# Performance work log

Hardware: AMD Instinct MI355X
Metric: run time of the kernel (lower is better)

Reference implementation:

```python
import jax, jax.numpy as jnp
import numpy as np


def setup_inputs() -> dict:
    key = jax.random.key(0)
    kx, kw = jax.random.split(key)
    B, IN, OUT = 8192, 1024, 4096
    x = jax.random.normal(kx, (B, IN), dtype=jnp.float32)
    # torch.rand -> uniform [0,1)
    weight = jax.random.uniform(kw, (IN, OUT), dtype=jnp.float32)
    return {"x": x, "weight": weight}


def reference(x, weight):
    # Faithful to: (x.unsqueeze(-1) - weight).pow(2).sum(-2)
    # i.e. out[b, o] = sum_i (x[b, i] - weight[i, o])**2
    # Computed via the squared-distance expansion to avoid the
    # (B, in, out) broadcast intermediate:
    x_sq = jnp.sum(x * x, axis=-1, keepdims=True)          # (B, 1)
    w_sq = jnp.sum(weight * weight, axis=0)                # (OUT,)
    cross = jnp.matmul(x, weight)                          # (B, OUT)
    return x_sq - 2.0 * cross + w_sq
```

## Files before the change

### kernel.cpp

```cpp
#include <hip/hip_runtime.h>
#include <cstdint>
#include <cstddef>

#define B_DIM   8192
#define IN_DIM  1024
#define OUT_DIM 4096
#define KT2     (IN_DIM / 64)

typedef __attribute__((ext_vector_type(8)))  int   i32x8;
typedef __attribute__((ext_vector_type(4)))  int   i32x4;
typedef __attribute__((ext_vector_type(16))) float f32x16;

__device__ __forceinline__ void async_copy16(const void* gptr, void* ldsptr) {
    __builtin_amdgcn_global_load_lds(
        (__attribute__((address_space(1))) void*)gptr,
        (__attribute__((address_space(3))) void*)ldsptr,
        16, 0, 0);
}

__device__ __forceinline__ int pack4_fp8(float a, float b, float c, float d) {
    int pk = __builtin_amdgcn_cvt_pk_fp8_f32(a, b, 0, false);
    pk = __builtin_amdgcn_cvt_pk_fp8_f32(c, d, pk, true);
    return pk;
}


__global__ __launch_bounds__(256) void quant_kernel(
    const float* __restrict__ x, const float* __restrict__ wgt,
    unsigned char* __restrict__ At, unsigned char* __restrict__ Bt,
    float* __restrict__ xsq2,
    float* __restrict__ wsq2)
{
    __shared__ float tile[256 * 33];
    __shared__ float red[4][32];

    const int t = threadIdx.x;
    const int w = t >> 6;
    const int l = t & 63;
    const int b = blockIdx.x;

    if (b < 512) {
        const int mt = b >> 1, kh = b & 1;
        const int m  = mt * 32 + (l & 31);
        float s = 0.0f;
        #pragma unroll
        for (int p = 0; p < 2; ++p) {
            const int kt2 = kh * 8 + w * 2 + p;
            const float* src = x + (size_t)m * IN_DIM + kt2 * 64 + (l >> 5) * 32;
            i32x4 lo, hi;
            #pragma unroll
            for (int j = 0; j < 4; ++j) {
                float4 v = ((const float4*)src)[j];
                s += v.x*v.x + v.y*v.y + v.z*v.z + v.w*v.w;
                lo[j] = pack4_fp8(v.x, v.y, v.z, v.w);
            }
            #pragma unroll
            for (int j = 0; j < 4; ++j) {
                float4 v = ((const float4*)src)[4 + j];
                s += v.x*v.x + v.y*v.y + v.z*v.z + v.w*v.w;
                hi[j] = pack4_fp8(v.x, v.y, v.z, v.w);
            }
            unsigned char* pan = At + ((size_t)mt * KT2 + kt2) * 2048;
            *(i32x4*)(pan + l * 16)        = lo;
            *(i32x4*)(pan + 1024 + l * 16) = hi;
        }
        s += __shfl_down(s, 32, 64);
        if (l < 32) red[w][l] = s;
        __syncthreads();
        if (t < 32)
            xsq2[kh * B_DIM + mt * 32 + t] =
                red[0][t] + red[1][t] + red[2][t] + red[3][t];
    } else {
        const int idx = b - 512;
        const int nt = idx & 127, q = idx >> 7, n0 = nt * 32;

        const int rbase = t >> 2, cg = (t & 3) * 8;
        #pragma unroll
        for (int rep = 0; rep < 4; ++rep) {
            const int r = rbase + rep * 64;
            const float* src = wgt + (size_t)(q * 256 + r) * OUT_DIM + n0 + cg;
            float4 v0 = ((const float4*)src)[0];
            float4 v1 = ((const float4*)src)[1];
            float* d = &tile[r * 33 + cg];
            d[0] = v0.x; d[1] = v0.y; d[2] = v0.z; d[3] = v0.w;
            d[4] = v1.x; d[5] = v1.y; d[6] = v1.z; d[7] = v1.w;
        }
        __syncthreads();

        const int kt2 = q * 4 + w;
        const int n   = l & 31;
        const int kb  = w * 64 + (l >> 5) * 32;
        float s = 0.0f;
        i32x4 lo, hi;
        #pragma unroll
        for (int j4 = 0; j4 < 4; ++j4) {
            float f0 = tile[(kb + j4 * 4 + 0) * 33 + n];
            float f1 = tile[(kb + j4 * 4 + 1) * 33 + n];
            float f2 = tile[(kb + j4 * 4 + 2) * 33 + n];
            float f3 = tile[(kb + j4 * 4 + 3) * 33 + n];
            s += f0*f0 + f1*f1 + f2*f2 + f3*f3;
            lo[j4] = pack4_fp8(f0, f1, f2, f3);
        }
        #pragma unroll
        for (int j4 = 0; j4 < 4; ++j4) {
            float f0 = tile[(kb + 16 + j4 * 4 + 0) * 33 + n];
            float f1 = tile[(kb + 16 + j4 * 4 + 1) * 33 + n];
            float f2 = tile[(kb + 16 + j4 * 4 + 2) * 33 + n];
            float f3 = tile[(kb + 16 + j4 * 4 + 3) * 33 + n];
            s += f0*f0 + f1*f1 + f2*f2 + f3*f3;
            hi[j4] = pack4_fp8(f0, f1, f2, f3);
        }
        unsigned char* pan = Bt + ((size_t)nt * KT2 + kt2) * 2048;
        *(i32x4*)(pan + l * 16)        = lo;
        *(i32x4*)(pan + 1024 + l * 16) = hi;

        s += __shfl_down(s, 32, 64);
        if (l < 32) red[w][l] = s;
        __syncthreads();
        if (t < 32)
            wsq2[q * OUT_DIM + n0 + t] =
                red[0][t] + red[1][t] + red[2][t] + red[3][t];
    }
}

__global__ __launch_bounds__(256, 2) void rbf_gemm_kernel(
    const unsigned char* __restrict__ At,
    const unsigned char* __restrict__ Bt,
    const float* __restrict__ xsq2,
    const float* __restrict__ wsq2,
    float* __restrict__ out)
{
    __shared__ __align__(16) unsigned char sm[73728];

    const int t    = threadIdx.x;
    const int w    = t >> 6;
    const int l    = t & 63;
    const int l32  = l & 31;
    const int half = l >> 5;

    const int wg  = blockIdx.y * 64 + blockIdx.x;
    const int x8  = wg & 7;
    const int i   = wg >> 3;
    const int bng = i >> 5;
    const int bmi = (i >> 2) & 7;
    const int bm  = x8 * 8 + bmi;
    const int bn  = bng * 4 + (i & 3);

    f32x16 acc[4][2];
    #pragma unroll
    for (int mi = 0; mi < 4; ++mi)
        #pragma unroll
        for (int ni = 0; ni < 2; ++ni)
            #pragma unroll
            for (int r = 0; r < 16; ++r)
                acc[mi][ni][r] = 0.0f;

    const unsigned char* gaBase  = At + (size_t)(bm * 4 + w)      * (KT2 * 2048);
    const unsigned char* gbBase0 = Bt + (size_t)(bn * 8 + w * 2)  * (KT2 * 2048);
    const unsigned char* gbBase1 = gbBase0 + (size_t)(KT2 * 2048);

    auto stage = [&](int buf, int k) {
        unsigned char* As = sm + buf * 24576;
        unsigned char* Bs = As + 8192;
        const unsigned char* ga  = gaBase  + k * 2048;
        const unsigned char* gb0 = gbBase0 + k * 2048;
        const unsigned char* gb1 = gbBase1 + k * 2048;
        #pragma unroll
        for (int h = 0; h < 2; ++h) {
            async_copy16(ga  + h * 1024 + l * 16, As + w * 2048 + h * 1024);
            async_copy16(gb0 + h * 1024 + l * 16, Bs + (w * 2 + 0) * 2048 + h * 1024);
            async_copy16(gb1 + h * 1024 + l * 16, Bs + (w * 2 + 1) * 2048 + h * 1024);
        }
    };

    auto ldfrag = [&](const unsigned char* base, int p) -> i32x8 {
        i32x4 lo = *(const i32x4*)(base + p * 2048 + l * 16);
        i32x4 hi = *(const i32x4*)(base + p * 2048 + 1024 + l * 16);
        i32x8 r;
        r[0] = lo[0]; r[1] = lo[1]; r[2] = lo[2]; r[3] = lo[3];
        r[4] = hi[0]; r[5] = hi[1]; r[6] = hi[2]; r[7] = hi[3];
        return r;
    };

    stage(0, 0);
    stage(1, 1);

    int cb = 0, sb = 2;
    for (int k = 0; k < 16; ++k) {
        if (k < 15) asm volatile("s_waitcnt vmcnt(6)" ::: "memory");
        else        asm volatile("s_waitcnt vmcnt(0)" ::: "memory");
        __builtin_amdgcn_s_barrier();
        __builtin_amdgcn_sched_barrier(0);

        if (k <= 13) stage(sb, k + 2);

        const unsigned char* As = sm + cb * 24576;
        const unsigned char* Bs = As + 8192;
        i32x8 bf0 = ldfrag(Bs, w * 2 + 0);
        i32x8 bf1 = ldfrag(Bs, w * 2 + 1);
        i32x8 af[4];
        #pragma unroll
        for (int mi = 0; mi < 4; ++mi)
            af[mi] = ldfrag(As, mi);

        __builtin_amdgcn_s_setprio(1);
        #pragma unroll
        for (int mi = 0; mi < 4; ++mi) {
            acc[mi][0] = __builtin_amdgcn_mfma_scale_f32_32x32x64_f8f6f4(
                af[mi], bf0, acc[mi][0],
                0, 0,
                0, 0x7F7F7F7F,
                0, 0x7F7F7F7F);
            acc[mi][1] = __builtin_amdgcn_mfma_scale_f32_32x32x64_f8f6f4(
                af[mi], bf1, acc[mi][1],
                0, 0, 0, 0x7F7F7F7F, 0, 0x7F7F7F7F);
        }
        __builtin_amdgcn_s_setprio(0);

        cb = (cb == 2) ? 0 : cb + 1;
        sb = (sb == 2) ? 0 : sb + 1;
    }

    const int ncol = bn * 256 + w * 64 + l32;
    const float wsn0 = wsq2[ncol]      + wsq2[OUT_DIM + ncol]
                     + wsq2[2 * OUT_DIM + ncol]      + wsq2[3 * OUT_DIM + ncol];
    const float wsn1 = wsq2[ncol + 32] + wsq2[OUT_DIM + ncol + 32]
                     + wsq2[2 * OUT_DIM + ncol + 32] + wsq2[3 * OUT_DIM + ncol + 32];
    #pragma unroll
    for (int mi = 0; mi < 4; ++mi) {
        const int mbase = bm * 128 + mi * 32 + 4 * half;
        #pragma unroll
        for (int r2 = 0; r2 < 4; ++r2) {
            #pragma unroll
            for (int r1 = 0; r1 < 4; ++r1) {
                const int m  = mbase + r1 + 8 * r2;
                const float xs = xsq2[m] + xsq2[B_DIM + m];
                float* orow = out + (size_t)m * OUT_DIM + ncol;
                orow[0]  = xs + wsn0 - 2.0f * acc[mi][0][r2 * 4 + r1];
                orow[32] = xs + wsn1 - 2.0f * acc[mi][1][r2 * 4 + r1];
            }
        }
    }
}

extern "C" void kernel_launch(void* const* d_in, const int* in_sizes, int n_in,
                              void* d_out, int out_size, void* d_ws, size_t ws_size,
                              hipStream_t stream)
{
    const float* x   = (const float*)d_in[0];
    const float* wgt = (const float*)d_in[1];
    float* out = (float*)d_out;
    char*  ws  = (char*)d_ws;

    unsigned char* At = (unsigned char*)ws;
    unsigned char* Bt = (unsigned char*)(ws + (size_t)B_DIM * IN_DIM);
    float* xsq2 = (float*)(ws + (size_t)B_DIM * IN_DIM + (size_t)OUT_DIM * IN_DIM);
    float* wsq2 = xsq2 + 2 * B_DIM;

    quant_kernel<<<1024, 256, 0, stream>>>(x, wgt, At, Bt, xsq2, wsq2);
    rbf_gemm_kernel<<<dim3(64, 16), 256, 0, stream>>>(At, Bt, xsq2, wsq2, out);
}
```

Measured before the change: 192.4 us.

## Load per-wave B fragments straight into registers instead of staging through LDS

Each wave uses only its own two B fragments, so the kernel now loads them directly from global memory into double-buffered registers rather than staging them through shared memory. Only the A tile keeps the three-slot async LDS pipeline, which cuts shared memory from 72KB to 24KB. The k-loop is fully unrolled so register buffer slots resolve statically, and the vmcnt waits are adjusted for the new load counts. In exchange, B gets only one iteration of prefetch lookahead instead of two, and register pressure rises.

```diff
diff --git a/kernel.cpp b/kernel.cpp
--- a/kernel.cpp
+++ b/kernel.cpp
@@ -130,7 +130,7 @@
     const float* __restrict__ wsq2,
     float* __restrict__ out)
 {
-    __shared__ __align__(16) unsigned char sm[73728];
+    __shared__ __align__(16) unsigned char sm[3][8192];
 
     const int t    = threadIdx.x;
     const int w    = t >> 6;
@@ -155,25 +155,20 @@
             for (int r = 0; r < 16; ++r)
                 acc[mi][ni][r] = 0.0f;
 
-    const unsigned char* gaBase  = At + (size_t)(bm * 4 + w)      * (KT2 * 2048);
-    const unsigned char* gbBase0 = Bt + (size_t)(bn * 8 + w * 2)  * (KT2 * 2048);
+    const unsigned char* gaBase  = At + (size_t)(bm * 4 + w)     * (KT2 * 2048);
+    const unsigned char* gbBase0 = Bt + (size_t)(bn * 8 + w * 2) * (KT2 * 2048);
     const unsigned char* gbBase1 = gbBase0 + (size_t)(KT2 * 2048);
 
-    auto stage = [&](int buf, int k) {
-        unsigned char* As = sm + buf * 24576;
-        unsigned char* Bs = As + 8192;
-        const unsigned char* ga  = gaBase  + k * 2048;
-        const unsigned char* gb0 = gbBase0 + k * 2048;
-        const unsigned char* gb1 = gbBase1 + k * 2048;
-        #pragma unroll
-        for (int h = 0; h < 2; ++h) {
-            async_copy16(ga  + h * 1024 + l * 16, As + w * 2048 + h * 1024);
-            async_copy16(gb0 + h * 1024 + l * 16, Bs + (w * 2 + 0) * 2048 + h * 1024);
-            async_copy16(gb1 + h * 1024 + l * 16, Bs + (w * 2 + 1) * 2048 + h * 1024);
-        }
+    i32x4 bq[2][2][2];
+
+    auto stageA = [&](int buf, int k) {
+        const unsigned char* ga = gaBase + k * 2048;
+        unsigned char* As = (unsigned char*)sm + buf * 8192 + w * 2048;
+        async_copy16(ga + l * 16,        As);
+        async_copy16(ga + 1024 + l * 16, As + 1024);
     };
 
-    auto ldfrag = [&](const unsigned char* base, int p) -> i32x8 {
+    auto ldfragA = [&](const unsigned char* base, int p) -> i32x8 {
         i32x4 lo = *(const i32x4*)(base + p * 2048 + l * 16);
         i32x4 hi = *(const i32x4*)(base + p * 2048 + 1024 + l * 16);
         i32x8 r;
@@ -182,26 +177,50 @@
         return r;
     };
 
-    stage(0, 0);
-    stage(1, 1);
-
-    int cb = 0, sb = 2;
+    stageA(0, 0);
+    {
+        const unsigned char* g0 = gbBase0;
+        const unsigned char* g1 = gbBase1;
+        bq[0][0][0] = *(const i32x4*)(g0 + l * 16);
+        bq[0][0][1] = *(const i32x4*)(g0 + 1024 + l * 16);
+        bq[0][1][0] = *(const i32x4*)(g1 + l * 16);
+        bq[0][1][1] = *(const i32x4*)(g1 + 1024 + l * 16);
+    }
+    stageA(1, 1);
+
+    #pragma unroll
     for (int k = 0; k < 16; ++k) {
-        if (k < 15) asm volatile("s_waitcnt vmcnt(6)" ::: "memory");
+        if (k < 15) asm volatile("s_waitcnt vmcnt(2)" ::: "memory");
         else        asm volatile("s_waitcnt vmcnt(0)" ::: "memory");
         __builtin_amdgcn_s_barrier();
         __builtin_amdgcn_sched_barrier(0);
 
-        if (k <= 13) stage(sb, k + 2);
-
-        const unsigned char* As = sm + cb * 24576;
-        const unsigned char* Bs = As + 8192;
-        i32x8 bf0 = ldfrag(Bs, w * 2 + 0);
-        i32x8 bf1 = ldfrag(Bs, w * 2 + 1);
+        if (k <= 14) {
+            const int slot = (k + 1) & 1;
+            const unsigned char* g0 = gbBase0 + (k + 1) * 2048;
+            const unsigned char* g1 = gbBase1 + (k + 1) * 2048;
+            bq[slot][0][0] = *(const i32x4*)(g0 + l * 16);
+            bq[slot][0][1] = *(const i32x4*)(g0 + 1024 + l * 16);
+            bq[slot][1][0] = *(const i32x4*)(g1 + l * 16);
+            bq[slot][1][1] = *(const i32x4*)(g1 + 1024 + l * 16);
+        }
+        if (k <= 13) stageA((k + 2) % 3, k + 2);
+
+        const unsigned char* As = (const unsigned char*)sm + (k % 3) * 8192;
         i32x8 af[4];
         #pragma unroll
         for (int mi = 0; mi < 4; ++mi)
-            af[mi] = ldfrag(As, mi);
+            af[mi] = ldfragA(As, mi);
+
+        const int cs = k & 1;
+        i32x8 bf0, bf1;
+        #pragma unroll
+        for (int j = 0; j < 4; ++j) {
+            bf0[j]     = bq[cs][0][0][j];
+            bf0[4 + j] = bq[cs][0][1][j];
+            bf1[j]     = bq[cs][1][0][j];
+            bf1[4 + j] = bq[cs][1][1][j];
+        }
 
         __builtin_amdgcn_s_setprio(1);
         #pragma unroll
@@ -216,9 +235,6 @@
                 0, 0, 0, 0x7F7F7F7F, 0, 0x7F7F7F7F);
         }
         __builtin_amdgcn_s_setprio(0);
-
-        cb = (cb == 2) ? 0 : cb + 1;
-        sb = (sb == 2) ? 0 : sb + 1;
     }
 
     const int ncol = bn * 256 + w * 64 + l32;
```

Result: no change. 195.4 us (+1.6%).
